# Kernel tuning notes

Measured on AMD Instinct MI355X. Metric: run time of the kernel, lower is better.

## Reference

```python
import jax, jax.numpy as jnp
import numpy as np

N = 8192        # nodes
IN_F = 256      # in_features
OUT_F = 64      # out_features per head
HEADS = 4
ALPHA = 0.2     # leaky relu slope
NEG_INF = -9e15


def setup_inputs() -> dict:
    key = jax.random.key(0)
    ks = jax.random.split(key, 8)
    h = jax.random.normal(ks[0], (N, IN_F), dtype=jnp.float32)
    adj = jax.random.randint(ks[1], (N, N), 0, 2, dtype=jnp.int32)
    # per-head GAT params, stacked over heads
    W = jax.random.normal(ks[2], (HEADS, IN_F, OUT_F), dtype=jnp.float32) * (1.0 / np.sqrt(IN_F))
    a1 = jax.random.normal(ks[3], (HEADS, OUT_F), dtype=jnp.float32) * (1.0 / np.sqrt(OUT_F))
    a2 = jax.random.normal(ks[4], (HEADS, OUT_F), dtype=jnp.float32) * (1.0 / np.sqrt(OUT_F))
    # fusing linear: Linear(out*heads, out)
    fc_w = jax.random.normal(ks[5], (OUT_F, HEADS * OUT_F), dtype=jnp.float32) * (1.0 / np.sqrt(HEADS * OUT_F))
    fc_b = jax.random.normal(ks[6], (OUT_F,), dtype=jnp.float32) * 0.01
    return {"h": h, "adj": adj, "W": W, "a1": a1, "a2": a2, "fc_w": fc_w, "fc_b": fc_b}


def reference(h, adj, W, a1, a2, fc_w, fc_b):
    # all heads batched: Wh [H, N, F]
    Wh = jnp.einsum('ni,hio->hno', h, W)
    # attention logits e_ij = leakyrelu(a1.Wh_i + a2.Wh_j), shape [H, N, N]
    e_src = jnp.einsum('hno,ho->hn', Wh, a1)   # [H, N]
    e_dst = jnp.einsum('hno,ho->hn', Wh, a2)   # [H, N]
    e = jax.nn.leaky_relu(e_src[:, :, None] + e_dst[:, None, :], ALPHA)
    e = jnp.where(adj[None] > 0, e, NEG_INF)
    attn = jax.nn.softmax(e, axis=-1)          # masked softmax over neighbors
    out = jnp.einsum('hnm,hmo->hno', attn, Wh)  # [H, N, F]
    out = jax.nn.elu(out)
    # concat heads along feature dim -> [N, H*F], then fuse linear
    h_concat = jnp.transpose(out, (1, 0, 2)).reshape(N, HEADS * OUT_F)
    return h_concat @ fc_w.T + fc_b
```

## Files before the change

kernel.cpp:

```cpp
#include <hip/hip_runtime.h>
#include <hip/hip_bf16.h>

#define NN 8192
#define NHEADS 4
#define OUTF 64
#define NCHUNK 4
#define CHUNK 2048
#define ROWS 32
#define LOG2E 1.4426950408889634f

typedef __bf16 bf16x8 __attribute__((ext_vector_type(8)));
typedef float fx4 __attribute__((ext_vector_type(4)));
typedef int ix4 __attribute__((ext_vector_type(4)));
typedef unsigned short ushort8 __attribute__((ext_vector_type(8)));

__global__ __launch_bounds__(256) void k_wh(
    const float* __restrict__ h, const float* __restrict__ W,
    const float* __restrict__ a1, const float* __restrict__ a2,
    unsigned short* __restrict__ whsw, float* __restrict__ R,
    float* __restrict__ F1, float* __restrict__ F2)
{
  const int tid = threadIdx.x;
  const int bx = blockIdx.x;
  const int hd = bx >> 7;
  const int i0 = (bx & 127) << 6;
  const int w = tid >> 6, o = tid & 63;
  const int ibase = i0 + w * 16;

  float acc[16];
#pragma unroll
  for (int m = 0; m < 16; ++m) acc[m] = 0.f;

  const float* hp = h + (size_t)ibase * 256;
  const float* Wp = W + hd * (256 * 64) + o;
  for (int k4 = 0; k4 < 64; ++k4) {
    float w0 = Wp[(k4 * 4 + 0) * 64];
    float w1 = Wp[(k4 * 4 + 1) * 64];
    float w2 = Wp[(k4 * 4 + 2) * 64];
    float w3 = Wp[(k4 * 4 + 3) * 64];
#pragma unroll
    for (int m = 0; m < 16; ++m) {
      fx4 hv = *(const fx4*)(hp + m * 256 + k4 * 4);
      acc[m] += hv[0] * w0 + hv[1] * w1 + hv[2] * w2 + hv[3] * w3;
    }
  }

  const float a1v = a1[hd * 64 + o], a2v = a2[hd * 64 + o];
#pragma unroll
  for (int m = 0; m < 16; ++m) {
    float s1 = acc[m] * a1v, s2 = acc[m] * a2v;
#pragma unroll
    for (int d = 1; d < 64; d <<= 1) {
      s1 += __shfl_xor(s1, d);
      s2 += __shfl_xor(s2, d);
    }
    if (o == 0) {
      int ix = hd * NN + ibase + m;
      R[ix]  = __builtin_amdgcn_exp2f(-0.8f * s1 * LOG2E);
      F1[ix] = __builtin_amdgcn_exp2f(s2 * LOG2E);
      F2[ix] = __builtin_amdgcn_exp2f(0.2f * s2 * LOG2E);
    }
  }

  size_t base = (size_t)hd * 524288 + (size_t)((i0 >> 5) + (w >> 1)) * 2048 +
                (size_t)(o >> 4) * 512;
  int ln0 = (o & 15) + 16 * ((w & 1) * 2);
  ushort8 pk0, pk1;
#pragma unroll
  for (int m = 0; m < 8; ++m) {
    pk0[m] = __builtin_bit_cast(unsigned short, (__bf16)acc[m]);
    pk1[m] = __builtin_bit_cast(unsigned short, (__bf16)acc[m + 8]);
  }
  *(ushort8*)(whsw + base + (size_t)ln0 * 8) = pk0;
  *(ushort8*)(whsw + base + (size_t)(ln0 + 16) * 8) = pk1;
}

struct Tile {
  fx4 f1a, f1b, f2a, f2b;
  bf16x8 b0, b1, b2, b3;
  unsigned m0, m1;
};

__device__ __forceinline__ void load_tile(Tile& t, const float* F1p,
                                          const float* F2p,
                                          const unsigned short* wp,
                                          const unsigned* bml, int il, int jb)
{
  t.f1a = *(const fx4*)(F1p + jb);
  t.f1b = *(const fx4*)(F1p + jb + 4);
  t.f2a = *(const fx4*)(F2p + jb);
  t.f2b = *(const fx4*)(F2p + jb + 4);
  const unsigned short* wq = wp + (size_t)(jb >> 5) * 2048;
  t.b0 = *(const bf16x8*)(wq);
  t.b1 = *(const bf16x8*)(wq + 512);
  t.b2 = *(const bf16x8*)(wq + 1024);
  t.b3 = *(const bf16x8*)(wq + 1536);
  const unsigned* mb = bml + (jb >> 5) * 33;
  t.m0 = mb[il];
  t.m1 = mb[16 + il];
}

__device__ __forceinline__ void compute_tile(const Tile& t, const float* Rr,
                                             int g, const bf16x8& ones,
                                             fx4 acc[2][4], fx4* accS)
{
#pragma unroll
  for (int rs = 0; rs < 2; ++rs) {
    unsigned sm = (rs ? t.m1 : t.m0) >> (g * 8);
    float p[8];
#pragma unroll
    for (int e = 0; e < 8; ++e) {
      float f1 = (e < 4) ? t.f1a[e] : t.f1b[e - 4];
      float f2 = (e < 4) ? t.f2a[e] : t.f2b[e - 4];
      float pm = fmaxf(f1, Rr[rs] * f2);
      unsigned keep = (unsigned)(((int)(sm << (31 - e))) >> 31);
      p[e] = __builtin_bit_cast(float,
                 __builtin_bit_cast(unsigned, pm) & keep);
    }
    bf16x8 af;
#pragma unroll
    for (int e = 0; e < 8; ++e) af[e] = (__bf16)p[e];
    acc[rs][0] = __builtin_amdgcn_mfma_f32_16x16x32_bf16(af, t.b0, acc[rs][0], 0, 0, 0);
    acc[rs][1] = __builtin_amdgcn_mfma_f32_16x16x32_bf16(af, t.b1, acc[rs][1], 0, 0, 0);
    acc[rs][2] = __builtin_amdgcn_mfma_f32_16x16x32_bf16(af, t.b2, acc[rs][2], 0, 0, 0);
    acc[rs][3] = __builtin_amdgcn_mfma_f32_16x16x32_bf16(af, t.b3, acc[rs][3], 0, 0, 0);
    accS[rs] = __builtin_amdgcn_mfma_f32_16x16x32_bf16(af, ones, accS[rs], 0, 0, 0);
  }
}

__global__ __launch_bounds__(256) void k_attn(
    const int* __restrict__ adj, const unsigned short* __restrict__ whsw,
    const float* __restrict__ Rg, const float* __restrict__ F1g,
    const float* __restrict__ F2g, float* __restrict__ pacc,
    float* __restrict__ psum)
{
  __shared__ unsigned bml[(CHUNK / 32) * 33];
  const int tid = threadIdx.x;
  const int lane = tid & 63;
  const int hd = tid >> 6;
  const int bx = blockIdx.x;
  const int xcd = bx & 7;
  const int ci = xcd >> 1;
  const int rt = ((bx >> 3) << 1) | (xcd & 1);
  const int i0 = rt << 5;
  const int j0 = ci * CHUNK;
  const int il = lane & 15;
  const int g = lane >> 4;

  {
    const int* ap = adj + (size_t)(i0 + hd * 8) * NN + j0 + lane * 32;
    ix4 vA[8], vB[8];
#pragma unroll
    for (int u = 0; u < 8; ++u)
      vA[u] = *(const ix4*)(ap + u * 4);

#pragma unroll
    for (int i = 0; i < 8; ++i) {
      ix4* cur = (i & 1) ? vB : vA;
      ix4* nxt = (i & 1) ? vA : vB;
      if (i < 7) {
        const int* np = ap + (size_t)(i + 1) * NN;
#pragma unroll
        for (int u = 0; u < 8; ++u)
          nxt[u] = *(const ix4*)(np + u * 4);
      }
      unsigned wrd = 0;
#pragma unroll
      for (int u = 0; u < 8; ++u) {
        wrd |= ((unsigned)cur[u][0]) << (u * 4 + 0);
        wrd |= ((unsigned)cur[u][1]) << (u * 4 + 1);
        wrd |= ((unsigned)cur[u][2]) << (u * 4 + 2);
        wrd |= ((unsigned)cur[u][3]) << (u * 4 + 3);
      }
      bml[lane * 33 + hd * 8 + i] = wrd;
    }
  }
  __syncthreads();

  float Rr[2];
#pragma unroll
  for (int rs = 0; rs < 2; ++rs)
    Rr[rs] = Rg[hd * NN + i0 + rs * 16 + il];
  const float* F1p = F1g + hd * NN + j0 + g * 8;
  const float* F2p = F2g + hd * NN + j0 + g * 8;
  const unsigned short* wp = whsw + (size_t)hd * 524288 +
                             (size_t)(j0 >> 5) * 2048 + (size_t)lane * 8;
  bf16x8 ones;
#pragma unroll
  for (int e = 0; e < 8; ++e) ones[e] = (__bf16)1.0f;

  fx4 acc[2][4] = {};
  fx4 accS[2] = {};

  Tile t0, t1;
  load_tile(t0, F1p, F2p, wp, bml, il, 0);
  for (int jb = 0; jb < CHUNK; jb += 64) {
    load_tile(t1, F1p, F2p, wp, bml, il, jb + 32);
    compute_tile(t0, Rr, g, ones, acc, accS);
    if (jb + 64 < CHUNK) load_tile(t0, F1p, F2p, wp, bml, il, jb + 64);
    compute_tile(t1, Rr, g, ones, acc, accS);
  }

#pragma unroll
  for (int rs = 0; rs < 2; ++rs) {
    if (il == 0) {
#pragma unroll
      for (int r = 0; r < 4; ++r)
        psum[(size_t)(ci * NHEADS + hd) * NN + i0 + rs * 16 + g * 4 + r] =
            accS[rs][r];
    }
  }

  float* pc = pacc + (size_t)ci * NN * 256;
#pragma unroll
  for (int rs = 0; rs < 2; ++rs)
#pragma unroll
    for (int r = 0; r < 4; ++r)
#pragma unroll
      for (int ft = 0; ft < 4; ++ft)
        pc[(size_t)(i0 + rs * 16 + g * 4 + r) * 256 + hd * 64 + ft * 16 + il] =
            acc[rs][ft][r];
}

__global__ __launch_bounds__(256) void k_fc(
    const float* __restrict__ pacc, const float* __restrict__ psum,
    const float* __restrict__ fcw, const float* __restrict__ fcb,
    float* __restrict__ out)
{
  __shared__ float ws[256 * 65];
  __shared__ float ash[32 * 260];
  __shared__ float inv[32 * 4];
  const int tid = threadIdx.x;
  const int i0 = blockIdx.x * 32;

  for (int idx = tid; idx < 64 * 256; idx += 256) {
    int o = idx >> 8, c = idx & 255;
    ws[c * 65 + o] = fcw[idx];
  }
  if (tid < 128) {
    int m = tid >> 2, hh = tid & 3;
    float s = 0.f;
#pragma unroll
    for (int ci = 0; ci < NCHUNK; ++ci)
      s += psum[(size_t)(ci * NHEADS + hh) * NN + i0 + m];
    inv[m * 4 + hh] = 1.0f / s;
  }
  __syncthreads();

  for (int idx = tid; idx < 32 * 64; idx += 256) {
    int m = idx >> 6, q = idx & 63;
    int hh = q >> 4;
    size_t off = (size_t)(i0 + m) * 256 + q * 4;
    fx4 v = {};
#pragma unroll
    for (int ci = 0; ci < NCHUNK; ++ci) {
      fx4 a = *(const fx4*)(pacc + (size_t)ci * NN * 256 + off);
      v[0] += a[0]; v[1] += a[1]; v[2] += a[2]; v[3] += a[3];
    }
    float iv = inv[m * 4 + hh];
#pragma unroll
    for (int j = 0; j < 4; ++j) {
      float x = v[j] * iv;
      x = (x > 0.f) ? x : (__builtin_amdgcn_exp2f(x * LOG2E) - 1.0f);
      ash[m * 260 + q * 4 + j] = x;
    }
  }
  __syncthreads();

  const int w = tid >> 6, o = tid & 63;
  float acc[8];
#pragma unroll
  for (int m = 0; m < 8; ++m) acc[m] = 0.f;

  for (int c4 = 0; c4 < 64; ++c4) {
    float w0 = ws[(c4 * 4 + 0) * 65 + o];
    float w1 = ws[(c4 * 4 + 1) * 65 + o];
    float w2 = ws[(c4 * 4 + 2) * 65 + o];
    float w3 = ws[(c4 * 4 + 3) * 65 + o];
#pragma unroll
    for (int m = 0; m < 8; ++m) {
      fx4 hv = *(const fx4*)(&ash[(w * 8 + m) * 260 + c4 * 4]);
      acc[m] += hv[0] * w0 + hv[1] * w1 + hv[2] * w2 + hv[3] * w3;
    }
  }
  const float bo = fcb[o];
#pragma unroll
  for (int m = 0; m < 8; ++m)
    out[(size_t)(i0 + w * 8 + m) * 64 + o] = acc[m] + bo;
}

extern "C" void kernel_launch(void* const* d_in, const int* in_sizes, int n_in,
                              void* d_out, int out_size, void* d_ws, size_t ws_size,
                              hipStream_t stream) {
  (void)in_sizes; (void)n_in; (void)out_size; (void)ws_size;
  const float* h   = (const float*)d_in[0];
  const int*   adj = (const int*)d_in[1];
  const float* W   = (const float*)d_in[2];
  const float* a1  = (const float*)d_in[3];
  const float* a2  = (const float*)d_in[4];
  const float* fcw = (const float*)d_in[5];
  const float* fcb = (const float*)d_in[6];
  float* out = (float*)d_out;

  char* base = (char*)d_ws;
  unsigned short* whsw = (unsigned short*)base;
  float* R  = (float*)(base + (4u << 20));
  float* F1 = (float*)(base + (4u << 20) + (128u << 10));
  float* F2 = (float*)(base + (4u << 20) + (256u << 10));
  float* pacc = (float*)(base + (5u << 20));
  float* psum = (float*)(base + (37u << 20));

  k_wh<<<dim3(512), dim3(256), 0, stream>>>(h, W, a1, a2, whsw, R, F1, F2);
  k_attn<<<dim3(1024), dim3(256), 0, stream>>>(adj, whsw, R, F1, F2, pacc, psum);
  k_fc<<<dim3(256), dim3(256), 0, stream>>>(pacc, psum, fcw, fcb, out);
}
```

Measured before the change: 252.8 us.

## Store partial attention accumulators in bf16, stage W in LDS, pre-transpose fc weights

The per-chunk partial accumulators written by the attention kernel are now bf16 instead of fp32, halving the 32 MB intermediate write and read between k_attn and k_fc. k_wh stages each head's W slice in shared memory so it can be read as vectors, and an extra block transposes fc_w once into the workspace. k_fc then reads the transposed weights from global memory instead of rebuilding a 64 KB LDS copy in every block. Rounding the partial sums to bf16 before the cross-chunk sum and normalisation costs some accuracy.

```diff
diff --git a/kernel.cpp b/kernel.cpp
--- a/kernel.cpp
+++ b/kernel.cpp
@@ -3,10 +3,8 @@
 
 #define NN 8192
 #define NHEADS 4
-#define OUTF 64
 #define NCHUNK 4
 #define CHUNK 2048
-#define ROWS 32
 #define LOG2E 1.4426950408889634f
 
 typedef __bf16 bf16x8 __attribute__((ext_vector_type(8)));
@@ -14,34 +12,52 @@
 typedef int ix4 __attribute__((ext_vector_type(4)));
 typedef unsigned short ushort8 __attribute__((ext_vector_type(8)));
 
+__device__ __forceinline__ float bf2f(unsigned short u) {
+  return __builtin_bit_cast(float, ((unsigned)u) << 16);
+}
+
 __global__ __launch_bounds__(256) void k_wh(
     const float* __restrict__ h, const float* __restrict__ W,
     const float* __restrict__ a1, const float* __restrict__ a2,
-    unsigned short* __restrict__ whsw, float* __restrict__ R,
-    float* __restrict__ F1, float* __restrict__ F2)
-{
+    const float* __restrict__ fcw, unsigned short* __restrict__ whsw,
+    float* __restrict__ R, float* __restrict__ F1, float* __restrict__ F2,
+    float* __restrict__ fcwT)
+{
+  __shared__ float ws[64 * 260];
   const int tid = threadIdx.x;
   const int bx = blockIdx.x;
+
+  if (bx == 512) {
+    for (int idx = tid; idx < 64 * 256; idx += 256) {
+      int o = idx >> 8, c = idx & 255;
+      fcwT[c * 64 + o] = fcw[o * 256 + c];
+    }
+    return;
+  }
+
   const int hd = bx >> 7;
   const int i0 = (bx & 127) << 6;
+
+  const float* Wp = W + hd * (256 * 64);
+  for (int idx = tid; idx < 256 * 64; idx += 256) {
+    int k = idx >> 6, o = idx & 63;
+    ws[o * 260 + k] = Wp[idx];
+  }
+  __syncthreads();
+
   const int w = tid >> 6, o = tid & 63;
   const int ibase = i0 + w * 16;
-
   float acc[16];
 #pragma unroll
   for (int m = 0; m < 16; ++m) acc[m] = 0.f;
 
   const float* hp = h + (size_t)ibase * 256;
-  const float* Wp = W + hd * (256 * 64) + o;
   for (int k4 = 0; k4 < 64; ++k4) {
-    float w0 = Wp[(k4 * 4 + 0) * 64];
-    float w1 = Wp[(k4 * 4 + 1) * 64];
-    float w2 = Wp[(k4 * 4 + 2) * 64];
-    float w3 = Wp[(k4 * 4 + 3) * 64];
+    fx4 wv = *(const fx4*)(&ws[o * 260 + k4 * 4]);
 #pragma unroll
     for (int m = 0; m < 16; ++m) {
       fx4 hv = *(const fx4*)(hp + m * 256 + k4 * 4);
-      acc[m] += hv[0] * w0 + hv[1] * w1 + hv[2] * w2 + hv[3] * w3;
+      acc[m] += hv[0] * wv[0] + hv[1] * wv[1] + hv[2] * wv[2] + hv[3] * wv[3];
     }
   }
 
@@ -131,7 +147,7 @@
 __global__ __launch_bounds__(256) void k_attn(
     const int* __restrict__ adj, const unsigned short* __restrict__ whsw,
     const float* __restrict__ Rg, const float* __restrict__ F1g,
-    const float* __restrict__ F2g, float* __restrict__ pacc,
+    const float* __restrict__ F2g, unsigned short* __restrict__ paccB,
     float* __restrict__ psum)
 {
   __shared__ unsigned bml[(CHUNK / 32) * 33];
@@ -211,7 +227,7 @@
     }
   }
 
-  float* pc = pacc + (size_t)ci * NN * 256;
+  unsigned short* pc = paccB + (size_t)ci * NN * 256;
 #pragma unroll
   for (int rs = 0; rs < 2; ++rs)
 #pragma unroll
@@ -219,24 +235,19 @@
 #pragma unroll
       for (int ft = 0; ft < 4; ++ft)
         pc[(size_t)(i0 + rs * 16 + g * 4 + r) * 256 + hd * 64 + ft * 16 + il] =
-            acc[rs][ft][r];
+            __builtin_bit_cast(unsigned short, (__bf16)acc[rs][ft][r]);
 }
 
 __global__ __launch_bounds__(256) void k_fc(
-    const float* __restrict__ pacc, const float* __restrict__ psum,
-    const float* __restrict__ fcw, const float* __restrict__ fcb,
+    const unsigned short* __restrict__ paccB, const float* __restrict__ psum,
+    const float* __restrict__ fcwT, const float* __restrict__ fcb,
     float* __restrict__ out)
 {
-  __shared__ float ws[256 * 65];
   __shared__ float ash[32 * 260];
   __shared__ float inv[32 * 4];
   const int tid = threadIdx.x;
   const int i0 = blockIdx.x * 32;
 
-  for (int idx = tid; idx < 64 * 256; idx += 256) {
-    int o = idx >> 8, c = idx & 255;
-    ws[c * 65 + o] = fcw[idx];
-  }
   if (tid < 128) {
     int m = tid >> 2, hh = tid & 3;
     float s = 0.f;
@@ -247,22 +258,22 @@
   }
   __syncthreads();
 
-  for (int idx = tid; idx < 32 * 64; idx += 256) {
-    int m = idx >> 6, q = idx & 63;
-    int hh = q >> 4;
-    size_t off = (size_t)(i0 + m) * 256 + q * 4;
-    fx4 v = {};
+  for (int idx = tid; idx < 32 * 32; idx += 256) {
+    int m = idx & 31, c8 = idx >> 5;
+    size_t off = ((size_t)(i0 + m)) * 256 + c8 * 8;
+    float v[8] = {0.f, 0.f, 0.f, 0.f, 0.f, 0.f, 0.f, 0.f};
 #pragma unroll
     for (int ci = 0; ci < NCHUNK; ++ci) {
-      fx4 a = *(const fx4*)(pacc + (size_t)ci * NN * 256 + off);
-      v[0] += a[0]; v[1] += a[1]; v[2] += a[2]; v[3] += a[3];
-    }
-    float iv = inv[m * 4 + hh];
-#pragma unroll
-    for (int j = 0; j < 4; ++j) {
+      ushort8 a = *(const ushort8*)(paccB + (size_t)ci * NN * 256 + off);
+#pragma unroll
+      for (int j = 0; j < 8; ++j) v[j] += bf2f(a[j]);
+    }
+    float iv = inv[m * 4 + (c8 >> 3)];
+#pragma unroll
+    for (int j = 0; j < 8; ++j) {
       float x = v[j] * iv;
       x = (x > 0.f) ? x : (__builtin_amdgcn_exp2f(x * LOG2E) - 1.0f);
-      ash[m * 260 + q * 4 + j] = x;
+      ash[m * 260 + c8 * 8 + j] = x;
     }
   }
   __syncthreads();
@@ -273,10 +284,10 @@
   for (int m = 0; m < 8; ++m) acc[m] = 0.f;
 
   for (int c4 = 0; c4 < 64; ++c4) {
-    float w0 = ws[(c4 * 4 + 0) * 65 + o];
-    float w1 = ws[(c4 * 4 + 1) * 65 + o];
-    float w2 = ws[(c4 * 4 + 2) * 65 + o];
-    float w3 = ws[(c4 * 4 + 3) * 65 + o];
+    float w0 = fcwT[(c4 * 4 + 0) * 64 + o];
+    float w1 = fcwT[(c4 * 4 + 1) * 64 + o];
+    float w2 = fcwT[(c4 * 4 + 2) * 64 + o];
+    float w3 = fcwT[(c4 * 4 + 3) * 64 + o];
 #pragma unroll
     for (int m = 0; m < 8; ++m) {
       fx4 hv = *(const fx4*)(&ash[(w * 8 + m) * 260 + c4 * 4]);
@@ -307,10 +318,11 @@
   float* R  = (float*)(base + (4u << 20));
   float* F1 = (float*)(base + (4u << 20) + (128u << 10));
   float* F2 = (float*)(base + (4u << 20) + (256u << 10));
-  float* pacc = (float*)(base + (5u << 20));
-  float* psum = (float*)(base + (37u << 20));
-
-  k_wh<<<dim3(512), dim3(256), 0, stream>>>(h, W, a1, a2, whsw, R, F1, F2);
-  k_attn<<<dim3(1024), dim3(256), 0, stream>>>(adj, whsw, R, F1, F2, pacc, psum);
-  k_fc<<<dim3(256), dim3(256), 0, stream>>>(pacc, psum, fcw, fcb, out);
-}
+  float* psum = (float*)(base + (5u << 20));
+  float* fcwT = (float*)(base + (6u << 20));
+  unsigned short* paccB = (unsigned short*)(base + (7u << 20));
+
+  k_wh<<<dim3(513), dim3(256), 0, stream>>>(h, W, a1, a2, fcw, whsw, R, F1, F2, fcwT);
+  k_attn<<<dim3(1024), dim3(256), 0, stream>>>(adj, whsw, R, F1, F2, paccB, psum);
+  k_fc<<<dim3(256), dim3(256), 0, stream>>>(paccB, psum, fcwT, fcb, out);
+}
```

Result: no change. 248.9 us (-1.6%).
